# Kernel optimization log

Measured on AMD Instinct MI355X. Metric: run time of the kernel, lower is better.

## Reference

```python
import jax, jax.numpy as jnp
from jax import lax
import numpy as np

CODEBOOK_SIZE = 512
VQ_DIM = 32


def _conv(x, w, b):
    # NCHW conv, 3x3, stride 1, SAME padding (padding=1 in torch)
    y = lax.conv_general_dilated(x, w, (1, 1), 'SAME',
                                 dimension_numbers=('NCHW', 'OIHW', 'NCHW'))
    return y + b[None, :, None, None]


def _maxpool2(x):
    return lax.reduce_window(x, -jnp.inf, lax.max, (1, 1, 2, 2), (1, 1, 2, 2), 'VALID')


def _upsample2(x):
    return jnp.repeat(jnp.repeat(x, 2, axis=2), 2, axis=3)


def _vq(x_flat, codebook):
    # x_flat: [b, n, d]; codebook: [K, d]
    # squared euclidean distances via expansion (avoids [b,n,K,d] tensor)
    x2 = jnp.sum(x_flat * x_flat, axis=-1, keepdims=True)          # [b,n,1]
    c2 = jnp.sum(codebook * codebook, axis=-1)                     # [K]
    xc = jnp.einsum('bnd,kd->bnk', x_flat, codebook)               # [b,n,K]
    dist = x2 - 2.0 * xc + c2[None, None, :]
    indices = jnp.argmin(dist, axis=-1)                            # [b,n] int
    quantized = codebook[indices]                                  # [b,n,d]
    # commitment loss (codebook treated as non-grad target, EMA-style)
    commit_loss = jnp.mean((jax.lax.stop_gradient(quantized) - x_flat) ** 2)
    # straight-through estimator
    quantized = x_flat + jax.lax.stop_gradient(quantized - x_flat)
    return quantized, indices, commit_loss


def _forward(x, w1, b1, w2, b2, codebook, w3, b3, w4, b4):
    h = _conv(x, w1, b1)            # [b,16,256,256]
    h = _maxpool2(h)                # [b,16,128,128]
    h = jax.nn.gelu(h, approximate=False)
    h = _conv(h, w2, b2)            # [b,32,128,128]
    h = _maxpool2(h)                # [b,32,64,64]
    b, c, H, W = h.shape
    h_flat = jnp.transpose(h, (0, 2, 3, 1)).reshape(b, H * W, c)   # b (h w) c
    q, indices, commit_loss = _vq(h_flat, codebook)
    h = jnp.transpose(q.reshape(b, H, W, c), (0, 3, 1, 2))         # [b,32,64,64]
    h = _upsample2(h)               # [b,32,128,128]
    h = _conv(h, w3, b3)            # [b,16,128,128]
    h = jax.nn.gelu(h, approximate=False)
    h = _upsample2(h)               # [b,16,256,256]
    h = _conv(h, w4, b4)            # [b,1,256,256]
    return jnp.clip(h, -1.0, 1.0), indices, commit_loss


def setup_inputs() -> dict:
    key = jax.random.key(0)
    ks = jax.random.split(key, 10)
    def w(k, shape):
        fan_in = int(np.prod(shape[1:]))
        return jax.random.normal(k, shape, dtype=jnp.float32) * (1.0 / np.sqrt(fan_in))
    return {
        'x': jax.random.normal(ks[0], (64, 1, 256, 256), dtype=jnp.float32),
        'w1': w(ks[1], (16, 1, 3, 3)),  'b1': jnp.zeros((16,), jnp.float32),
        'w2': w(ks[2], (32, 16, 3, 3)), 'b2': jnp.zeros((32,), jnp.float32),
        'codebook': jax.random.normal(ks[3], (CODEBOOK_SIZE, VQ_DIM), dtype=jnp.float32),
        'w3': w(ks[4], (16, 32, 3, 3)), 'b3': jnp.zeros((16,), jnp.float32),
        'w4': w(ks[5], (1, 16, 3, 3)),  'b4': jnp.zeros((1,), jnp.float32),
    }


def reference(x, w1, b1, w2, b2, codebook, w3, b3, w4, b4):
    return _forward(x, w1, b1, w2, b2, codebook, w3, b3, w4, b4)
```

## Files before the change

kernel.cpp:

```cpp
#include <hip/hip_runtime.h>
#include <math.h>


#define GELUF(v) (0.5f * (v) * (1.0f + erff((v) * 0.70710678118654752440f)))
#define MAXFLAG 262144

typedef __attribute__((ext_vector_type(8))) short short8;
typedef __attribute__((ext_vector_type(4))) float float4v;

static __device__ inline unsigned short f2bf(float f) {
    unsigned u = __float_as_uint(f);
    unsigned r = (u + 0x7FFFu + ((u >> 16) & 1u)) >> 16;
    return (unsigned short)r;
}
static __device__ inline float bf2f(unsigned short h) {
    return __uint_as_float(((unsigned)h) << 16);
}

__global__ __launch_bounds__(256) void k_conv1t(const float* __restrict__ x,
                                                const float* __restrict__ w1,
                                                const float* __restrict__ b1,
                                                unsigned short* __restrict__ h1h,
                                                unsigned short* __restrict__ h1l) {
    __shared__ float s_x[34 * 36];

    int tid = threadIdx.x;
    int n = blockIdx.x >> 6;
    int tile = blockIdx.x & 63;
    int ty = tile >> 3, tx = tile & 7;
    const float* xin = x + (size_t)n * 65536;

    int gy0 = 32 * ty - 1, gx0 = 32 * tx - 1;
    for (int e = tid; e < 1156; e += 256) {
        int r = e / 34, c = e - r * 34;
        int gy = gy0 + r, gx = gx0 + c;
        float v = 0.0f;
        if (gy >= 0 && gy < 256 && gx >= 0 && gx < 256)
            v = xin[gy * 256 + gx];
        s_x[r * 36 + c] = v;
    }
    __syncthreads();

    int ly = tid >> 4, lx = tid & 15;
    float patch[4][4];
    const float* sp = s_x + (2 * ly) * 36 + 2 * lx;
#pragma unroll
    for (int i = 0; i < 4; i++)
#pragma unroll
        for (int j = 0; j < 4; j++)
            patch[i][j] = sp[i * 36 + j];

    unsigned short hi[16], lo[16];
#pragma unroll
    for (int c = 0; c < 16; c++) {
        float m = -INFINITY;
#pragma unroll
        for (int sy = 0; sy < 2; sy++)
#pragma unroll
            for (int sx = 0; sx < 2; sx++) {
                float acc = b1[c];
#pragma unroll
                for (int ky = 0; ky < 3; ky++)
#pragma unroll
                    for (int kx = 0; kx < 3; kx++)
                        acc += w1[c * 9 + ky * 3 + kx] * patch[sy + ky][sx + kx];
                m = fmaxf(m, acc);
            }
        float g = GELUF(m);
        hi[c] = f2bf(g);
        lo[c] = f2bf(g - bf2f(hi[c]));
    }

    int yo = 16 * ty + ly, xo = 16 * tx + lx;
    size_t off = ((size_t)((n << 14) + (yo << 7) + xo)) << 4;
    uint ph[8], pl[8];
#pragma unroll
    for (int c2 = 0; c2 < 8; c2++) {
        ph[c2] = (uint)hi[2 * c2] | ((uint)hi[2 * c2 + 1] << 16);
        pl[c2] = (uint)lo[2 * c2] | ((uint)lo[2 * c2 + 1] << 16);
    }
    uint4* dh = (uint4*)(h1h + off);
    uint4* dl = (uint4*)(h1l + off);
    dh[0] = make_uint4(ph[0], ph[1], ph[2], ph[3]);
    dh[1] = make_uint4(ph[4], ph[5], ph[6], ph[7]);
    dl[0] = make_uint4(pl[0], pl[1], pl[2], pl[3]);
    dl[1] = make_uint4(pl[4], pl[5], pl[6], pl[7]);
}

__global__ __launch_bounds__(256) void k_conv2m(const unsigned short* __restrict__ h1h,
                                                const unsigned short* __restrict__ h1l,
                                                const unsigned short* __restrict__ w2h,
                                                const unsigned short* __restrict__ w2l,
                                                const float* __restrict__ b2,
                                                float* __restrict__ h2) {
    __shared__ unsigned short s_hi[18 * 2 * 18 * 8];
    __shared__ unsigned short s_lo[18 * 2 * 18 * 8];
    __shared__ unsigned short s_wh[32 * 10 * 2 * 8];
    __shared__ unsigned short s_wl[32 * 10 * 2 * 8];
    __shared__ float s_pool[32 * 64];

    int tid = threadIdx.x;
    int n = blockIdx.x >> 6;
    int tile = blockIdx.x & 63;
    int cx0 = (tile & 7) << 4, cy0 = (tile >> 3) << 4;

    {
        const uint* gh = (const uint*)w2h;
        const uint* gl = (const uint*)w2l;
        uint* dh = (uint*)s_wh; uint* dl = (uint*)s_wl;
        for (int e = tid; e < 2560; e += 256) { dh[e] = gh[e]; dl[e] = gl[e]; }
    }
    {
        const uint* gh = (const uint*)(h1h + (((size_t)n) << 18));
        const uint* gl = (const uint*)(h1l + (((size_t)n) << 18));
        uint* dh = (uint*)s_hi; uint* dl = (uint*)s_lo;
        for (int e = tid; e < 2592; e += 256) {
            int r = e / 144;
            int rem = e - r * 144;
            int c = rem >> 3;
            int dw = rem & 7;
            int y = cy0 - 1 + r, xx = cx0 - 1 + c;
            uint vh = 0, vl = 0;
            if (y >= 0 && y < 128 && xx >= 0 && xx < 128) {
                size_t g = ((size_t)((y << 7) + xx) << 3) + dw;
                vh = gh[g]; vl = gl[g];
            }
            int half = dw >> 2;
            int du = (((r * 2 + half) * 18 + c) << 2) + (dw & 3);
            dh[du] = vh; dl[du] = vl;
        }
    }
    __syncthreads();

    int lane = tid & 63, wid = tid >> 6;
    int m = lane & 15, quad = lane >> 4;
    int tl = quad >> 1, half = quad & 1;

    float4v acc[4][2];
#pragma unroll
    for (int mt = 0; mt < 4; mt++)
#pragma unroll
        for (int nt = 0; nt < 2; nt++)
            acc[mt][nt] = (float4v){0.0f, 0.0f, 0.0f, 0.0f};

    for (int s = 0; s < 5; s++) {
        int tA = (s < 4) ? (2 * s + tl) : 8;
        int tB = (s < 4) ? (2 * s + tl) : (8 + tl);
        short8 Bh[2], Bl[2];
#pragma unroll
        for (int nt = 0; nt < 2; nt++) {
            int u = ((nt * 16 + m) * 10 + tB) * 2 + half;
            Bh[nt] = *(const short8*)(s_wh + (u << 3));
            Bl[nt] = *(const short8*)(s_wl + (u << 3));
        }
        int ky = tA / 3, kx = tA - 3 * (tA / 3);
        short8 Ah[4], Al[4];
#pragma unroll
        for (int mt = 0; mt < 4; mt++) {
            int u = (((wid * 4 + mt + ky) * 2 + half) * 18) + m + kx;
            Ah[mt] = *(const short8*)(s_hi + (u << 3));
            Al[mt] = *(const short8*)(s_lo + (u << 3));
        }
#pragma unroll
        for (int mt = 0; mt < 4; mt++)
#pragma unroll
            for (int nt = 0; nt < 2; nt++) {
                float4v z = acc[mt][nt];
                z = __builtin_amdgcn_mfma_f32_16x16x32_bf16(Al[mt], Bh[nt], z, 0, 0, 0);
                z = __builtin_amdgcn_mfma_f32_16x16x32_bf16(Ah[mt], Bl[nt], z, 0, 0, 0);
                z = __builtin_amdgcn_mfma_f32_16x16x32_bf16(Ah[mt], Bh[nt], z, 0, 0, 0);
                acc[mt][nt] = z;
            }
    }

#pragma unroll
    for (int nt = 0; nt < 2; nt++) {
        int cout = nt * 16 + m;
        float bias = b2[cout];
#pragma unroll
        for (int mtp = 0; mtp < 2; mtp++) {
            float4v a0 = acc[2 * mtp][nt], a1 = acc[2 * mtp + 1][nt];
            float p0 = fmaxf(fmaxf(a0[0], a0[1]), fmaxf(a1[0], a1[1])) + bias;
            float p1 = fmaxf(fmaxf(a0[2], a0[3]), fmaxf(a1[2], a1[3])) + bias;
            int py = wid * 2 + mtp;
            int px = quad * 2;
            s_pool[cout * 64 + py * 8 + px]     = p0;
            s_pool[cout * 64 + py * 8 + px + 1] = p1;
        }
    }
    __syncthreads();
    {
        int c = tid >> 3, pr = tid & 7;
        float* dst = h2 + (((size_t)(n * 32 + c)) << 12) + ((cy0 >> 1) + pr) * 64 + (cx0 >> 1);
        const float4* src = (const float4*)(s_pool + c * 64 + pr * 8);
        ((float4*)dst)[0] = src[0];
        ((float4*)dst)[1] = src[1];
    }
}

__global__ __launch_bounds__(256) void k_vq_mfma(const float* __restrict__ h2,
                                                 const unsigned short* __restrict__ cbh,
                                                 const unsigned short* __restrict__ cbl,
                                                 const float* __restrict__ c2g,
                                                 float* __restrict__ idx_out,
                                                 float* __restrict__ loss_out,
                                                 int* __restrict__ nflag,
                                                 int* __restrict__ flags) {
    __shared__ float s_best[256], s_best2[256];
    __shared__ int   s_bi[256];
    __shared__ float wsum[4];

    int tid = threadIdx.x;
    int lane = tid & 63;
    int wid  = tid >> 6;
    int m    = lane & 15;
    int quad = lane >> 4;

    int img = blockIdx.x >> 4;
    int sp0 = (blockIdx.x & 15) << 8;
    const float* xb = h2 + ((size_t)(img * 32) << 12) + sp0;

    short8 Ahi[4], Alo[4];
    float x2r[4][4];
    float x2own[4];
#pragma unroll
    for (int mt = 0; mt < 4; mt++) {
        const float* xp = xb + wid * 64 + mt * 16 + m;
        float x2 = 0.0f;
#pragma unroll
        for (int j = 0; j < 8; j++) {
            float fe = xp[(size_t)(quad * 8 + j) << 12];
            x2 += fe * fe;
            unsigned short hi = f2bf(fe);
            unsigned short lo = f2bf(fe - bf2f(hi));
            Ahi[mt][j] = (short)hi;
            Alo[mt][j] = (short)lo;
        }
        x2 += __shfl_xor(x2, 16);
        x2 += __shfl_xor(x2, 32);
        x2own[mt] = x2;
    }
#pragma unroll
    for (int mt = 0; mt < 4; mt++)
#pragma unroll
        for (int r = 0; r < 4; r++)
            x2r[mt][r] = __shfl(x2own[mt], quad * 4 + r);

    float best[4][4], best2[4][4];
    int bi[4][4];
#pragma unroll
    for (int mt = 0; mt < 4; mt++)
#pragma unroll
        for (int r = 0; r < 4; r++) {
            best[mt][r] = INFINITY; best2[mt][r] = INFINITY; bi[mt][r] = 0;
        }

    size_t boff = ((size_t)m << 5) + (quad << 3);
    short8 Bh = *(const short8*)(cbh + boff);
    short8 Bl = *(const short8*)(cbl + boff);
    float  c2v = c2g[m];

    for (int nt = 0; nt < 32; nt++) {
        short8 curBh = Bh, curBl = Bl;
        float  curc2 = c2v;
        if (nt < 31) {
            size_t o = boff + ((size_t)(nt + 1) << 9);
            Bh = *(const short8*)(cbh + o);
            Bl = *(const short8*)(cbl + o);
            c2v = c2g[(nt + 1) * 16 + m];
        }
        int ncode = nt * 16 + m;

        float4v acc[4];
#pragma unroll
        for (int mt = 0; mt < 4; mt++) {
            float4v z = {0.0f, 0.0f, 0.0f, 0.0f};
            z = __builtin_amdgcn_mfma_f32_16x16x32_bf16(Alo[mt], curBh, z, 0, 0, 0);
            z = __builtin_amdgcn_mfma_f32_16x16x32_bf16(Ahi[mt], curBl, z, 0, 0, 0);
            z = __builtin_amdgcn_mfma_f32_16x16x32_bf16(Ahi[mt], curBh, z, 0, 0, 0);
            acc[mt] = z;
        }
#pragma unroll
        for (int mt = 0; mt < 4; mt++)
#pragma unroll
            for (int r = 0; r < 4; r++) {
                float dist = fmaf(acc[mt][r], -2.0f, curc2);
                best2[mt][r] = fminf(best2[mt][r], fmaxf(dist, best[mt][r]));
                bool lt = dist < best[mt][r];
                bi[mt][r] = lt ? ncode : bi[mt][r];
                best[mt][r] = fminf(best[mt][r], dist);
            }
    }

#pragma unroll
    for (int mt = 0; mt < 4; mt++)
#pragma unroll
        for (int r = 0; r < 4; r++) {
            float b1v = best[mt][r], b2v = best2[mt][r];
            int   biv = bi[mt][r];
#pragma unroll
            for (int mask = 1; mask < 16; mask <<= 1) {
                float ob = __shfl_xor(b1v, mask);
                float ob2 = __shfl_xor(b2v, mask);
                int   obi = __shfl_xor(biv, mask);
                b2v = fminf(fminf(b2v, ob2), fmaxf(b1v, ob));
                if (ob < b1v || (ob == b1v && obi < biv)) { b1v = ob; biv = obi; }
            }
            if (m == 0) {
                int p = wid * 64 + mt * 16 + quad * 4 + r;
                s_best[p] = b1v + x2r[mt][r];
                s_best2[p] = b2v + x2r[mt][r];
                s_bi[p] = biv;
            }
        }
    __syncthreads();

    int pos = blockIdx.x * 256 + tid;
    float bb = s_best[tid], bb2 = s_best2[tid];
    int   kk = s_bi[tid];
    idx_out[pos] = (float)kk;

    float eps = 0.02f + 0.0005f * fabsf(bb);
    if (bb2 - bb < eps) {
        int slot = atomicAdd(nflag, 1);
        if (slot < MAXFLAG) flags[slot] = pos;
    }

    float lsum = fmaxf(bb, 0.0f);
#pragma unroll
    for (int o = 32; o > 0; o >>= 1) lsum += __shfl_down(lsum, o);
    if (lane == 0) wsum[wid] = lsum;
    __syncthreads();
    if (tid == 0)
        atomicAdd(loss_out, (wsum[0] + wsum[1] + wsum[2] + wsum[3]) * (1.0f / 8388608.0f));
}

__global__ __launch_bounds__(256) void k_lut(const float* __restrict__ wc3,
                                             const float* __restrict__ cb,
                                             float* __restrict__ lut) {
    int code = blockIdx.x;
    int t = threadIdx.x;
    float s = 0.0f;
    if (code < 512) {
        int pp = t >> 6, rem = t & 63;
        const float* wp = wc3 + pp * 2048 + rem;
        const float* cr = cb + code * 32;
        for (int cin = 0; cin < 32; cin++)
            s += wp[cin * 64] * cr[cin];
    }
    lut[(size_t)code * 256 + t] = s;
}

__global__ __launch_bounds__(64) void k_repair(const float* __restrict__ x,
                                               const float* __restrict__ w1,
                                               const float* __restrict__ b1,
                                               const float* __restrict__ w2,
                                               const float* __restrict__ b2,
                                               const float* __restrict__ cb,
                                               float* __restrict__ idx_out,
                                               const int* __restrict__ nflag,
                                               const int* __restrict__ flags) {
    __shared__ double h1w[16][16];
    __shared__ double xvd[32];
    int lane = threadIdx.x;
    int cnt = *nflag;
    if (cnt > MAXFLAG) cnt = MAXFLAG;

    for (int fi = blockIdx.x; fi < cnt; fi += gridDim.x) {
        int pos = flags[fi];
        int n = pos >> 12, sp = pos & 4095, yo = sp >> 6, xo = sp & 63;

        int pix = lane >> 2, cg = lane & 3;
        int dy = pix >> 2, dx = pix & 3;
        int yh = 2 * yo - 1 + dy, xh = 2 * xo - 1 + dx;
        double hv[4] = {0.0, 0.0, 0.0, 0.0};
        if (yh >= 0 && yh < 128 && xh >= 0 && xh < 128) {
            const float* xin = x + (size_t)n * 65536;
            double patch[4][4];
            int y0 = 2 * yh - 1, x0 = 2 * xh - 1;
#pragma unroll
            for (int i = 0; i < 4; i++) {
                int iy = y0 + i;
                bool oy = (iy >= 0 && iy < 256);
#pragma unroll
                for (int j = 0; j < 4; j++) {
                    int ix = x0 + j;
                    patch[i][j] = (oy && ix >= 0 && ix < 256) ? (double)xin[iy * 256 + ix] : 0.0;
                }
            }
#pragma unroll
            for (int j = 0; j < 4; j++) {
                int c = cg * 4 + j;
                double mm = -INFINITY;
#pragma unroll
                for (int sy = 0; sy < 2; sy++)
#pragma unroll
                    for (int sx = 0; sx < 2; sx++) {
                        double acc = (double)b1[c];
#pragma unroll
                        for (int ky = 0; ky < 3; ky++)
#pragma unroll
                            for (int kx = 0; kx < 3; kx++)
                                acc += (double)w1[c * 9 + ky * 3 + kx] * patch[sy + ky][sx + kx];
                        mm = fmax(mm, acc);
                    }
                hv[j] = 0.5 * mm * (1.0 + erf(mm * 0.70710678118654752440));
            }
        }
        __syncthreads();
#pragma unroll
        for (int j = 0; j < 4; j++) h1w[cg * 4 + j][pix] = hv[j];
        __syncthreads();

        if (lane < 32) {
            double bb = (double)b2[lane];
            double acc[2][2] = {{bb, bb}, {bb, bb}};
            for (int cin = 0; cin < 16; cin++)
#pragma unroll
                for (int ky = 0; ky < 3; ky++)
#pragma unroll
                    for (int kx = 0; kx < 3; kx++) {
                        double wv = (double)w2[((lane * 16 + cin) * 3 + ky) * 3 + kx];
#pragma unroll
                        for (int sy = 0; sy < 2; sy++)
#pragma unroll
                            for (int sx = 0; sx < 2; sx++)
                                acc[sy][sx] += wv * h1w[cin][(sy + ky) * 4 + (sx + kx)];
                    }
            xvd[lane] = fmax(fmax(acc[0][0], acc[0][1]), fmax(acc[1][0], acc[1][1]));
        }
        __syncthreads();

        double x2 = 0.0;
        for (int d = 0; d < 32; d++) x2 += xvd[d] * xvd[d];
        double best = INFINITY;
        int bi = 0;
        for (int j = 0; j < 8; j++) {
            int k = lane * 8 + j;
            const float* cp = cb + k * 32;
            double c2 = 0.0, dot = 0.0;
#pragma unroll
            for (int d = 0; d < 32; d++) {
                double cd = (double)cp[d];
                c2 += cd * cd;
                dot += xvd[d] * cd;
            }
            double dist = x2 - 2.0 * dot + c2;
            if (dist < best) { best = dist; bi = k; }
        }
#pragma unroll
        for (int o = 32; o > 0; o >>= 1) {
            double od = __shfl_down(best, o);
            int oi = __shfl_down(bi, o);
            if (od < best || (od == best && oi < bi)) { best = od; bi = oi; }
        }
        bi = __shfl(bi, 0);

        if (lane == 0) idx_out[(size_t)n * 4096 + sp] = (float)bi;
    }
}

__global__ __launch_bounds__(256) void k_prep(const float* __restrict__ w2,
                                              const float* __restrict__ w3,
                                              const float* __restrict__ w4,
                                              const float* __restrict__ cb,
                                              unsigned short* __restrict__ w2h,
                                              unsigned short* __restrict__ w2l,
                                              float* __restrict__ wc3,
                                              float* __restrict__ wc4,
                                              unsigned short* __restrict__ cbh,
                                              unsigned short* __restrict__ cbl,
                                              float* __restrict__ c2g) {
    const int masks[2][2] = {{1, 6}, {3, 4}};
    for (int e = threadIdx.x; e < 8192; e += 256) {
        int cout = e & 15, tap = (e >> 4) & 3, cin = (e >> 6) & 31, pp = e >> 11;
        int rm = masks[pp >> 1][tap >> 1], cm = masks[pp & 1][tap & 1];
        float s = 0.0f;
        for (int ky = 0; ky < 3; ky++)
            if ((rm >> ky) & 1)
                for (int kx = 0; kx < 3; kx++)
                    if ((cm >> kx) & 1) s += w3[(cout * 32 + cin) * 9 + ky * 3 + kx];
        wc3[e] = s;
    }
    for (int e = threadIdx.x; e < 1024; e += 256) {
        int tap = e & 3, cin = (e >> 2) & 15, pp = e >> 6;
        int rm = masks[pp >> 1][tap >> 1], cm = masks[pp & 1][tap & 1];
        float s = 0.0f;
        for (int ky = 0; ky < 3; ky++)
            if ((rm >> ky) & 1)
                for (int kx = 0; kx < 3; kx++)
                    if ((cm >> kx) & 1) s += w4[cin * 9 + ky * 3 + kx];
        wc4[e] = s;
    }
    for (int e = threadIdx.x; e < 5120; e += 256) {
        int cout = e / 160;
        int rem = e - cout * 160;
        int tap = rem >> 4;
        int cin = rem & 15;
        float v = 0.0f;
        if (tap < 9) {
            int ky = tap / 3, kx = tap - 3 * (tap / 3);
            v = w2[((cout * 16 + cin) * 3 + ky) * 3 + kx];
        }
        unsigned short hi = f2bf(v);
        unsigned short lo = f2bf(v - bf2f(hi));
        w2h[e] = hi;
        w2l[e] = lo;
    }
    for (int e = threadIdx.x; e < 16384; e += 256) {
        float v = cb[e];
        unsigned short hi = f2bf(v);
        cbh[e] = hi;
        cbl[e] = f2bf(v - bf2f(hi));
    }
    for (int k = threadIdx.x; k < 512; k += 256) {
        float c2 = 0.0f;
#pragma unroll
        for (int d = 0; d < 32; d++) {
            float fe = cb[k * 32 + d];
            c2 += fe * fe;
        }
        c2g[k] = c2;
    }
}

__global__ __launch_bounds__(256) void k_dec(const float* __restrict__ idxf,
                                             const float* __restrict__ lut,
                                             const float* __restrict__ b3,
                                             const float* __restrict__ wc4,
                                             const float* __restrict__ b4,
                                             float* __restrict__ out) {
    __shared__ int   s_code[11 * 11];
    __shared__ float s_h3[16 * 324];

    int tid = threadIdx.x;
    int n = blockIdx.x >> 6;
    int tile = blockIdx.x & 63;
    int ty = tile >> 3, tx = tile & 7;

    if (tid < 121) {
        int row = tid / 11, col = tid - row * 11;
        int ca = 8 * ty - 1 + row, cbx = 8 * tx - 1 + col;
        int code = 512;
        if (ca >= 0 && ca < 64 && cbx >= 0 && cbx < 64)
            code = (int)idxf[((size_t)n << 12) + (ca << 6) + cbx];
        s_code[tid] = code;
    }
    __syncthreads();

    for (int e = tid; e < 324; e += 256) {
        int r = e / 18, cc = e - r * 18;
        int Y = 16 * ty - 1 + r, X = 16 * tx - 1 + cc;
        float hv[16];
        if (Y >= 0 && Y < 128 && X >= 0 && X < 128) {
            int pp = ((Y & 1) << 1) | (X & 1);
            int la0 = (Y >> 1) - 1 + (Y & 1) - (8 * ty - 1);
            int lb0 = (X >> 1) - 1 + (X & 1) - (8 * tx - 1);
            float acc[16];
#pragma unroll
            for (int c = 0; c < 16; c++) acc[c] = b3[c];
#pragma unroll
            for (int dy = 0; dy < 2; dy++)
#pragma unroll
                for (int dx = 0; dx < 2; dx++) {
                    int code = s_code[(la0 + dy) * 11 + lb0 + dx];
                    const float4* lp = (const float4*)(lut + (size_t)code * 256 +
                                                       pp * 64 + (dy * 2 + dx) * 16);
#pragma unroll
                    for (int j = 0; j < 4; j++) {
                        float4 w = lp[j];
                        acc[4 * j + 0] += w.x;
                        acc[4 * j + 1] += w.y;
                        acc[4 * j + 2] += w.z;
                        acc[4 * j + 3] += w.w;
                    }
                }
#pragma unroll
            for (int c = 0; c < 16; c++) hv[c] = GELUF(acc[c]);
        } else {
#pragma unroll
            for (int c = 0; c < 16; c++) hv[c] = 0.0f;
        }
#pragma unroll
        for (int c = 0; c < 16; c++) s_h3[c * 324 + e] = hv[c];
    }
    __syncthreads();

    int ly = tid >> 4, lx = tid & 15;
    float bv = b4[0];
    float acc2[2][2] = {{bv, bv}, {bv, bv}};
    for (int cin = 0; cin < 16; cin++) {
        const float* hc = s_h3 + cin * 324;
        float v[3][3];
#pragma unroll
        for (int r = 0; r < 3; r++)
#pragma unroll
            for (int cc = 0; cc < 3; cc++)
                v[r][cc] = hc[(ly + r) * 18 + lx + cc];
#pragma unroll
        for (int py = 0; py < 2; py++)
#pragma unroll
            for (int px = 0; px < 2; px++)
#pragma unroll
                for (int dy = 0; dy < 2; dy++)
#pragma unroll
                    for (int dx = 0; dx < 2; dx++)
                        acc2[py][px] += wc4[(py * 2 + px) * 64 + cin * 4 + dy * 2 + dx] *
                                        v[py + dy][px + dx];
    }
    int a = 16 * ty + ly, b = 16 * tx + lx;
#pragma unroll
    for (int py = 0; py < 2; py++) {
        float2 f2 = make_float2(fminf(fmaxf(acc2[py][0], -1.0f), 1.0f),
                                fminf(fmaxf(acc2[py][1], -1.0f), 1.0f));
        *(float2*)(out + (size_t)n * 65536 + (2 * a + py) * 256 + 2 * b) = f2;
    }
}

extern "C" void kernel_launch(void* const* d_in, const int* in_sizes, int n_in,
                              void* d_out, int out_size, void* d_ws, size_t ws_size,
                              hipStream_t stream) {
    const float* x  = (const float*)d_in[0];
    const float* w1 = (const float*)d_in[1];
    const float* b1 = (const float*)d_in[2];
    const float* w2 = (const float*)d_in[3];
    const float* b2 = (const float*)d_in[4];
    const float* cb = (const float*)d_in[5];
    const float* w3 = (const float*)d_in[6];
    const float* b3 = (const float*)d_in[7];
    const float* w4 = (const float*)d_in[8];
    const float* b4 = (const float*)d_in[9];

    float* out      = (float*)d_out;
    float* idx_out  = out + 4194304;
    float* loss_out = out + 4194304 + 262144;

    char* ws = (char*)d_ws;
    unsigned short* h1h = (unsigned short*)ws;
    unsigned short* h1l = (unsigned short*)(ws + (size_t)33554432);
    float* h2  = (float*)(ws + (size_t)67108864);
    float* lut = (float*)(ws + (size_t)67108864);
    size_t T = 100663296;
    float* wc3 = (float*)(ws + T);
    float* wc4 = (float*)(ws + T + 32768);
    unsigned short* w2h = (unsigned short*)(ws + T + 36864);
    unsigned short* w2l = (unsigned short*)(ws + T + 47104);
    int* nflag = (int*)(ws + T + 57344);
    int* flags = (int*)(ws + T + 57408);
    size_t T2 = T + 57408 + 1048576;
    unsigned short* cbh = (unsigned short*)(ws + T2);
    unsigned short* cbl = (unsigned short*)(ws + T2 + 32768);
    float* c2g = (float*)(ws + T2 + 65536);

    (void)hipMemsetAsync(loss_out, 0, 4, stream);
    (void)hipMemsetAsync(nflag, 0, 4, stream);

    k_prep<<<1, 256, 0, stream>>>(w2, w3, w4, cb, w2h, w2l, wc3, wc4, cbh, cbl, c2g);
    k_conv1t<<<4096, 256, 0, stream>>>(x, w1, b1, h1h, h1l);
    k_conv2m<<<4096, 256, 0, stream>>>(h1h, h1l, w2h, w2l, b2, h2);
    k_vq_mfma<<<1024, 256, 0, stream>>>(h2, cbh, cbl, c2g, idx_out, loss_out, nflag, flags);
    k_lut<<<513, 256, 0, stream>>>(wc3, cb, lut);
    k_repair<<<16384, 64, 0, stream>>>(x, w1, b1, w2, b2, cb, idx_out, nflag, flags);
    k_dec<<<4096, 256, 0, stream>>>(idx_out, lut, b3, wc4, b4, out);
}
```

Measured before the change: 403.0 us.

## Fuse conv1+pool+gelu into conv2 kernel, recomputing halo in shared memory

Merges the first conv/maxpool/GELU stage into the conv2 MFMA kernel. Each block loads a 38x38 input patch and computes the 18x18 pooled h1 tile, halo included, directly into shared memory as bf16 hi/lo split. This removes the 64MB round trip of h1 hi/lo through global memory and one kernel launch. In exchange the halo is computed redundantly (324 vs 256 pixels per tile), and only 324 work items spread over 256 threads leaves the second pass poorly balanced.

```diff
diff --git a/kernel.cpp b/kernel.cpp
--- a/kernel.cpp
+++ b/kernel.cpp
@@ -17,87 +17,18 @@
     return __uint_as_float(((unsigned)h) << 16);
 }
 
-__global__ __launch_bounds__(256) void k_conv1t(const float* __restrict__ x,
-                                                const float* __restrict__ w1,
-                                                const float* __restrict__ b1,
-                                                unsigned short* __restrict__ h1h,
-                                                unsigned short* __restrict__ h1l) {
-    __shared__ float s_x[34 * 36];
-
-    int tid = threadIdx.x;
-    int n = blockIdx.x >> 6;
-    int tile = blockIdx.x & 63;
-    int ty = tile >> 3, tx = tile & 7;
-    const float* xin = x + (size_t)n * 65536;
-
-    int gy0 = 32 * ty - 1, gx0 = 32 * tx - 1;
-    for (int e = tid; e < 1156; e += 256) {
-        int r = e / 34, c = e - r * 34;
-        int gy = gy0 + r, gx = gx0 + c;
-        float v = 0.0f;
-        if (gy >= 0 && gy < 256 && gx >= 0 && gx < 256)
-            v = xin[gy * 256 + gx];
-        s_x[r * 36 + c] = v;
-    }
-    __syncthreads();
-
-    int ly = tid >> 4, lx = tid & 15;
-    float patch[4][4];
-    const float* sp = s_x + (2 * ly) * 36 + 2 * lx;
-#pragma unroll
-    for (int i = 0; i < 4; i++)
-#pragma unroll
-        for (int j = 0; j < 4; j++)
-            patch[i][j] = sp[i * 36 + j];
-
-    unsigned short hi[16], lo[16];
-#pragma unroll
-    for (int c = 0; c < 16; c++) {
-        float m = -INFINITY;
-#pragma unroll
-        for (int sy = 0; sy < 2; sy++)
-#pragma unroll
-            for (int sx = 0; sx < 2; sx++) {
-                float acc = b1[c];
-#pragma unroll
-                for (int ky = 0; ky < 3; ky++)
-#pragma unroll
-                    for (int kx = 0; kx < 3; kx++)
-                        acc += w1[c * 9 + ky * 3 + kx] * patch[sy + ky][sx + kx];
-                m = fmaxf(m, acc);
-            }
-        float g = GELUF(m);
-        hi[c] = f2bf(g);
-        lo[c] = f2bf(g - bf2f(hi[c]));
-    }
-
-    int yo = 16 * ty + ly, xo = 16 * tx + lx;
-    size_t off = ((size_t)((n << 14) + (yo << 7) + xo)) << 4;
-    uint ph[8], pl[8];
-#pragma unroll
-    for (int c2 = 0; c2 < 8; c2++) {
-        ph[c2] = (uint)hi[2 * c2] | ((uint)hi[2 * c2 + 1] << 16);
-        pl[c2] = (uint)lo[2 * c2] | ((uint)lo[2 * c2 + 1] << 16);
-    }
-    uint4* dh = (uint4*)(h1h + off);
-    uint4* dl = (uint4*)(h1l + off);
-    dh[0] = make_uint4(ph[0], ph[1], ph[2], ph[3]);
-    dh[1] = make_uint4(ph[4], ph[5], ph[6], ph[7]);
-    dl[0] = make_uint4(pl[0], pl[1], pl[2], pl[3]);
-    dl[1] = make_uint4(pl[4], pl[5], pl[6], pl[7]);
-}
-
-__global__ __launch_bounds__(256) void k_conv2m(const unsigned short* __restrict__ h1h,
-                                                const unsigned short* __restrict__ h1l,
-                                                const unsigned short* __restrict__ w2h,
-                                                const unsigned short* __restrict__ w2l,
-                                                const float* __restrict__ b2,
-                                                float* __restrict__ h2) {
+__global__ __launch_bounds__(256) void k_enc(const float* __restrict__ x,
+                                             const float* __restrict__ w1,
+                                             const float* __restrict__ b1,
+                                             const unsigned short* __restrict__ w2h,
+                                             const unsigned short* __restrict__ w2l,
+                                             const float* __restrict__ b2,
+                                             float* __restrict__ h2) {
+    __shared__ float s_scratch[2048];
     __shared__ unsigned short s_hi[18 * 2 * 18 * 8];
     __shared__ unsigned short s_lo[18 * 2 * 18 * 8];
-    __shared__ unsigned short s_wh[32 * 10 * 2 * 8];
-    __shared__ unsigned short s_wl[32 * 10 * 2 * 8];
-    __shared__ float s_pool[32 * 64];
+    __shared__ unsigned short s_wh[5120];
+    __shared__ unsigned short s_wl[5120];
 
     int tid = threadIdx.x;
     int n = blockIdx.x >> 6;
@@ -111,23 +42,65 @@
         for (int e = tid; e < 2560; e += 256) { dh[e] = gh[e]; dl[e] = gl[e]; }
     }
     {
-        const uint* gh = (const uint*)(h1h + (((size_t)n) << 18));
-        const uint* gl = (const uint*)(h1l + (((size_t)n) << 18));
-        uint* dh = (uint*)s_hi; uint* dl = (uint*)s_lo;
-        for (int e = tid; e < 2592; e += 256) {
-            int r = e / 144;
-            int rem = e - r * 144;
-            int c = rem >> 3;
-            int dw = rem & 7;
-            int y = cy0 - 1 + r, xx = cx0 - 1 + c;
-            uint vh = 0, vl = 0;
-            if (y >= 0 && y < 128 && xx >= 0 && xx < 128) {
-                size_t g = ((size_t)((y << 7) + xx) << 3) + dw;
-                vh = gh[g]; vl = gl[g];
-            }
+        const float* xin = x + (size_t)n * 65536;
+        int gy0 = 2 * cy0 - 3, gx0 = 2 * cx0 - 3;
+        for (int e = tid; e < 1444; e += 256) {
+            int r = e / 38, c = e - r * 38;
+            int gy = gy0 + r, gx = gx0 + c;
+            float v = 0.0f;
+            if (gy >= 0 && gy < 256 && gx >= 0 && gx < 256) v = xin[gy * 256 + gx];
+            s_scratch[r * 40 + c] = v;
+        }
+    }
+    __syncthreads();
+
+    for (int e = tid; e < 324; e += 256) {
+        int r = e / 18, c = e - r * 18;
+        int hy = cy0 - 1 + r, hx = cx0 - 1 + c;
+        uint ph[8], pl[8];
+        if (hy >= 0 && hy < 128 && hx >= 0 && hx < 128) {
+            float patch[4][4];
+            const float* sp = s_scratch + (2 * r) * 40 + 2 * c;
+#pragma unroll
+            for (int i = 0; i < 4; i++)
+#pragma unroll
+                for (int j = 0; j < 4; j++)
+                    patch[i][j] = sp[i * 40 + j];
+            unsigned short hi[16], lo[16];
+#pragma unroll
+            for (int ch = 0; ch < 16; ch++) {
+                float m = -INFINITY;
+#pragma unroll
+                for (int sy = 0; sy < 2; sy++)
+#pragma unroll
+                    for (int sx = 0; sx < 2; sx++) {
+                        float acc = b1[ch];
+#pragma unroll
+                        for (int ky = 0; ky < 3; ky++)
+#pragma unroll
+                            for (int kx = 0; kx < 3; kx++)
+                                acc += w1[ch * 9 + ky * 3 + kx] * patch[sy + ky][sx + kx];
+                        m = fmaxf(m, acc);
+                    }
+                float g = GELUF(m);
+                hi[ch] = f2bf(g);
+                lo[ch] = f2bf(g - bf2f(hi[ch]));
+            }
+#pragma unroll
+            for (int dw = 0; dw < 8; dw++) {
+                ph[dw] = (uint)hi[2 * dw] | ((uint)hi[2 * dw + 1] << 16);
+                pl[dw] = (uint)lo[2 * dw] | ((uint)lo[2 * dw + 1] << 16);
+            }
+        } else {
+#pragma unroll
+            for (int dw = 0; dw < 8; dw++) { ph[dw] = 0; pl[dw] = 0; }
+        }
+#pragma unroll
+        for (int dw = 0; dw < 8; dw++) {
             int half = dw >> 2;
             int du = (((r * 2 + half) * 18 + c) << 2) + (dw & 3);
-            dh[du] = vh; dl[du] = vl;
+            ((uint*)s_hi)[du] = ph[dw];
+            ((uint*)s_lo)[du] = pl[dw];
         }
     }
     __syncthreads();
@@ -173,6 +146,7 @@
             }
     }
 
+    float* s_pool = s_scratch;
 #pragma unroll
     for (int nt = 0; nt < 2; nt++) {
         int cout = nt * 16 + m;
@@ -636,8 +610,6 @@
     float* loss_out = out + 4194304 + 262144;
 
     char* ws = (char*)d_ws;
-    unsigned short* h1h = (unsigned short*)ws;
-    unsigned short* h1l = (unsigned short*)(ws + (size_t)33554432);
     float* h2  = (float*)(ws + (size_t)67108864);
     float* lut = (float*)(ws + (size_t)67108864);
     size_t T = 100663296;
@@ -656,8 +628,7 @@
     (void)hipMemsetAsync(nflag, 0, 4, stream);
 
     k_prep<<<1, 256, 0, stream>>>(w2, w3, w4, cb, w2h, w2l, wc3, wc4, cbh, cbl, c2g);
-    k_conv1t<<<4096, 256, 0, stream>>>(x, w1, b1, h1h, h1l);
-    k_conv2m<<<4096, 256, 0, stream>>>(h1h, h1l, w2h, w2l, b2, h2);
+    k_enc<<<4096, 256, 0, stream>>>(x, w1, b1, w2h, w2l, b2, h2);
     k_vq_mfma<<<1024, 256, 0, stream>>>(h2, cbh, cbl, c2g, idx_out, loss_out, nflag, flags);
     k_lut<<<513, 256, 0, stream>>>(wc3, cb, lut);
     k_repair<<<16384, 64, 0, stream>>>(x, w1, b1, w2, b2, cb, idx_out, nflag, flags);
```

Result: no change. 405.8 us (+0.7%).
